# Kernel tuning notes

Measured on AMD Instinct MI355X. Metric: run time of the kernel, lower is better.

## Reference

```python
import jax, jax.numpy as jnp
import numpy as np
from jax.scipy.special import logsumexp

N_NODES = 20000
N_FEAT = 64
N_TPL = 10
TPL_NODES = 10
K_NEIGH = 15  # local neighborhood cap -> local graph size kloc = K+1 (self first)
N_EDGES = N_NODES * 16


def setup_inputs() -> dict:
    key = jax.random.key(0)
    k1, k2, k3, k4, k5 = jax.random.split(key, 5)
    x = jax.random.normal(k1, (N_NODES, N_FEAT), dtype=jnp.float32)
    edge_index = jax.random.randint(k2, (2, N_EDGES), 0, N_NODES, dtype=jnp.int32)
    # template_initialisation: randint{0,1} adjacency + N(0, 0.01) noise
    adj = jax.random.randint(k3, (N_TPL, TPL_NODES, TPL_NODES), 0, 2).astype(jnp.float32)
    templates = adj + 0.01 * jax.random.normal(k4, (N_TPL, TPL_NODES, TPL_NODES), dtype=jnp.float32)
    # template features ~ N(0.0012, 0.02)
    templates_features = 0.0012 + 0.02 * jax.random.normal(
        k5, (N_TPL, TPL_NODES, N_FEAT), dtype=jnp.float32)
    alpha0 = jnp.array([0.5], dtype=jnp.float32)
    return {"x": x, "edge_index": edge_index, "templates": templates,
            "templates_features": templates_features, "alpha0": alpha0}


def _fgw_distances(x, edge_index, templates, templates_features, alpha0,
                   K=K_NEIGH, n_outer=3, n_sink=5):
    """Per-node fused GW distance between the node's local (star) subgraph and
    each learned template, solved with an entropic proximal / Sinkhorn scheme.
    Returns [N, T]."""
    N, F = x.shape
    Tn, n, _ = templates.shape
    kloc = K + 1

    # ---- build fixed-size neighbor lists from edge_index (int ops, constant) ----
    src, dst = edge_index[0], edge_index[1]
    E = src.shape[0]
    order = jnp.argsort(src)
    src_s, dst_s = src[order], dst[order]
    deg = jnp.zeros((N,), jnp.int32).at[src].add(1)
    start = jnp.cumsum(deg) - deg                       # CSR row starts
    rank = jnp.arange(E, dtype=jnp.int32) - start[src_s]  # position within each node's list
    # rank >= K falls out of bounds -> dropped
    neigh = jnp.zeros((N, K), jnp.int32).at[src_s, rank].set(dst_s, mode="drop")
    nb_mask = (jnp.arange(K)[None, :] < jnp.minimum(deg, K)[:, None]).astype(x.dtype)  # [N,K]

    # ---- local graphs: self node first, then up to K neighbors ----
    xloc = jnp.concatenate([x[:, None, :], x[neigh]], axis=1)  # [N, kloc, F]
    m = jnp.concatenate([jnp.ones((N, 1), x.dtype), nb_mask], axis=1)  # [N, kloc]
    p = m / jnp.sum(m, -1, keepdims=True)                # node-side marginal
    q = jnp.full((n,), 1.0 / n, x.dtype)                 # template-side marginal

    # star adjacency of the 1-hop neighborhood
    row0 = jnp.concatenate([jnp.zeros((N, 1), x.dtype), nb_mask], axis=1)
    C1 = jnp.zeros((N, kloc, kloc), x.dtype).at[:, 0, :].set(row0).at[:, :, 0].set(row0)
    C2 = templates  # [T, n, n]

    # feature cost M[n_node, t, k, m] = ||xloc - y||^2
    M = (jnp.sum(xloc ** 2, -1)[:, None, :, None]
         + jnp.sum(templates_features ** 2, -1)[None, :, None, :]
         - 2.0 * jnp.einsum("nkf,tmf->ntkm", xloc, templates_features))

    alpha = jax.nn.sigmoid(alpha0)[0]

    # GW square-loss constant terms (Peyre et al. trick)
    hC1 = jnp.einsum("nkl,nl->nk", C1 ** 2, p)   # [N, kloc]
    hC2 = jnp.einsum("tmr,r->tm", C2 ** 2, q)    # [T, n]
    constC = hC1[:, None, :, None] + hC2[None, :, None, :]

    def gw_tens(Tp):  # Tp: [N, T, kloc, n]
        tmp = jnp.einsum("nkl,ntlm->ntkm", C1, Tp)
        return constC - 2.0 * jnp.einsum("ntkm,trm->ntkr", tmp, C2)

    eps = 0.05 * jax.lax.stop_gradient(jnp.mean(M)) + 1e-6
    logp = jnp.where(m > 0, jnp.log(jnp.maximum(p, 1e-30)), -1e9)[:, None, :]  # [N,1,kloc]
    logq = jnp.log(q)  # [n]

    Tp = p[:, None, :, None] * q[None, None, None, :]  # independent-coupling init
    f = jnp.zeros((N, Tn, kloc), x.dtype)
    g = jnp.zeros((N, Tn, n), x.dtype)
    for _ in range(n_outer):  # outer FGW linearization steps
        G = (1.0 - alpha) * M + 2.0 * alpha * gw_tens(Tp)
        logK = -G / eps
        for _ in range(n_sink):  # log-domain Sinkhorn on linearized cost
            f = eps * (logp - logsumexp(logK + g[:, :, None, :] / eps, axis=-1))
            g = eps * (logq - logsumexp(logK + f[:, :, :, None] / eps, axis=-2))
        Tp = jnp.exp(logK + f[:, :, :, None] / eps + g[:, :, None, :] / eps)

    dist = ((1.0 - alpha) * jnp.sum(M * Tp, axis=(-2, -1))
            + alpha * jnp.sum(gw_tens(Tp) * Tp, axis=(-2, -1)))
    return dist  # [N, T]


def reference(x, edge_index, templates, templates_features, alpha0):
    return _fgw_distances(x, edge_index, templates, templates_features, alpha0)
```

## Files before the change

kernel.cpp:

```cpp
#include <hip/hip_runtime.h>

#define N_NODES 20000
#define NPAIRS  10000
#define N_EDGES 320000
#define CAP     64
#define KN      15

typedef _Float16 half_t;
typedef _Float16 half2_t __attribute__((ext_vector_type(2)));

#define P_ALPHA 0
#define P_BETA  1
#define P_IEPS2 2
#define P_EPS   3
#define P_HC2   16
#define P_RSC2  216
#define P_F1    316

#define OFF_CNT    0u
#define OFF_S2X    80000u
#define OFF_STATS  160000u
#define OFF_FLAG   160520u
#define OFF_NBC    160528u
#define OFF_NEIGH  240528u
#define OFF_BUF    1440528u
#define OFF_PARAMS 6560528u
#define MEMSET_LEN 160528u

#define TF_STRIDE 648

template<int CTRL>
__device__ __forceinline__ float dpp_add(float v) {
  int s = __builtin_bit_cast(int, v);
  int r = __builtin_amdgcn_update_dpp(0, s, CTRL, 0xF, 0xF, true);
  return v + __builtin_bit_cast(float, r);
}
__device__ __forceinline__ float sum16(float v) {
  v = dpp_add<0x128>(v);
  v = dpp_add<0x124>(v);
  v = dpp_add<0x122>(v);
  v = dpp_add<0x121>(v);
  return v;
}
__device__ __forceinline__ float bcast16(float v) {
  return __builtin_bit_cast(float,
      __builtin_amdgcn_ds_swizzle(__builtin_bit_cast(int, v), 0x010));
}
__device__ __forceinline__ float fdot2(half2_t a, half2_t b, float c) {
  return __builtin_amdgcn_fdot2(a, b, c, false);
}
__device__ __forceinline__ float sgpr(float v) {
  return __builtin_bit_cast(float,
      __builtin_amdgcn_readfirstlane(__builtin_bit_cast(int, v)));
}

__global__ void k_scatter(const int* __restrict__ ei, int* __restrict__ cnt,
                          int* __restrict__ buf) {
  int e = blockIdx.x * blockDim.x + threadIdx.x;
  if (e >= N_EDGES) return;
  int s = ei[e];
  int slot = atomicAdd(&cnt[s], 1);
  if (slot < CAP) buf[s * CAP + slot] = e;
}

#define SS_BLOCKS 1250
__global__ void __launch_bounds__(256)
k_selstats(const int* __restrict__ ei, const int* __restrict__ cnt,
           const int* __restrict__ buf, const float* __restrict__ x,
           int* __restrict__ nbc_g, int* __restrict__ neigh,
           float* __restrict__ s2xh, double* __restrict__ stats,
           int* __restrict__ flag,
           const float* __restrict__ tf, const float* __restrict__ c2,
           const float* __restrict__ alpha0, float* __restrict__ params) {
  const int lane = threadIdx.x & 63;
  const int wid = threadIdx.x >> 6;
  const int* dst = ei + N_EDGES;
  const float x0 = x[lane];
  const float x0sq = x0 * x0;
  float accx = 0.f, acc2 = 0.f;
  __shared__ int dsh[4][16];

  for (int w = blockIdx.x * 4 + wid; w < N_NODES; w += SS_BLOCKS * 4) {
    int c = cnt[w];
    int cc = c < CAP ? c : CAP;
    int e = (lane < cc) ? buf[w * CAP + lane] : 0x7fffffff;
    int nb = c < KN ? c : KN;
    bool sel;
    if (cc <= KN) {
      sel = lane < cc;
    } else {
      int rank = 0;
      for (int j = 0; j < cc; j++) {
        int ej = __shfl(e, j);
        rank += (ej < e) ? 1 : 0;
      }
      sel = (e != 0x7fffffff) && (rank < KN);
    }
    unsigned long long mask = __ballot(sel);
    int d = sel ? dst[e] : 0;
    if (sel) {
      int pos = __popcll(mask & ((1ull << lane) - 1ull));
      neigh[w * KN + pos] = d;
      dsh[wid][pos] = d;
    }
    if (lane == 0) nbc_g[w] = nb;

    float sv = x[w * 64 + lane];
    {
      float hv = (float)(half_t)sv;
      float sq = hv * hv;
#pragma unroll
      for (int off = 32; off > 0; off >>= 1) sq += __shfl_xor(sq, off, 64);
      if (lane == 0) s2xh[w] = sq;
    }
    float ax = sv, a2 = sv * sv;
    int idx[KN];
#pragma unroll
    for (int r = 0; r < KN; r++) idx[r] = dsh[wid][r];
#pragma unroll
    for (int r = 0; r < KN; r++) {
      if (r < nb) {
        float nv = x[(size_t)idx[r] * 64 + lane];
        ax += nv;
        a2 = fmaf(nv, nv, a2);
      }
    }
    float w0 = (float)(KN - nb);
    ax = fmaf(w0, x0, ax);
    a2 = fmaf(w0, x0sq, a2);
    accx += ax;
    acc2 += a2;
  }

#pragma unroll
  for (int off = 32; off > 0; off >>= 1) acc2 += __shfl_xor(acc2, off, 64);
  __shared__ float redx[4][64];
  __shared__ float red2[4];
  __shared__ int lastsh;
  redx[wid][lane] = accx;
  if (lane == 0) red2[wid] = acc2;
  __syncthreads();
  int tid = threadIdx.x;
  if (tid < 64) {
    float s = redx[0][tid] + redx[1][tid] + redx[2][tid] + redx[3][tid];
    atomicAdd(&stats[1 + tid], (double)s);
  }
  if (tid == 0)
    atomicAdd(&stats[0], (double)(red2[0] + red2[1] + red2[2] + red2[3]));
  __syncthreads();
  if (tid == 0) {
    __threadfence();
    int old = atomicAdd(flag, 1);
    lastsh = (old == SS_BLOCKS - 1) ? 1 : 0;
  }
  __syncthreads();
  if (!lastsh) return;
  __threadfence();
  __shared__ float sh[4];
  if (tid < 64) {
    float s = 0.f, s2 = 0.f;
    for (int tm = 0; tm < 100; tm++) { float v = tf[tm * 64 + tid]; s += v; s2 += v * v; }
    double inv16N = 1.0 / (double)(N_NODES * 16);
    double cross = (stats[1 + tid] * inv16N) * ((double)s / 100.0);
    double B = (double)s2 / 100.0;
    double term = B - 2.0 * cross;
#pragma unroll
    for (int off = 32; off > 0; off >>= 1) term += __shfl_xor(term, off, 64);
    if (tid == 0) {
      double A = stats[0] * inv16N;
      double meanM = A + term;
      float eps = (float)(0.05 * meanM) + 1e-6f;
      float a0 = alpha0[0];
      float alpha = 1.f / (1.f + expf(-a0));
      params[P_ALPHA] = alpha;
      params[P_BETA]  = 1.f - alpha;
      params[P_IEPS2] = 1.4426950408889634f / eps;
      params[P_EPS]   = eps;
      sh[0] = alpha; sh[1] = 1.f - alpha; sh[2] = 1.4426950408889634f / eps;
    }
  }
  __syncthreads();
  if (tid < 100) {
    float alpha = sh[0], beta = sh[1], ieps2 = sh[2];
    int t = tid / 10, mm = tid % 10;
    float h = 0.f;
    for (int r = 0; r < 10; r++) { float cv = c2[t * 100 + mm * 10 + r]; h += cv * cv; }
    float hc2v = 0.1f * h;
    params[P_HC2 + tid] = hc2v;
    float s2 = 0.f;
    for (int f = 0; f < 64; f++) { float v = tf[tid * 64 + f]; s2 += v * v; }
    float rs = 0.f;
    for (int m2_ = 0; m2_ < 10; m2_++) rs += c2[t * 100 + mm * 10 + m2_];
    params[P_RSC2 + tid] = rs;
    params[P_F1 + tid] = (beta * s2 + 2.0f * alpha * hc2v) * (-ieps2);
  }
}

__global__ void __launch_bounds__(320, 6)
k_main(const float* __restrict__ x, const float* __restrict__ tf_g,
       const float* __restrict__ c2_g, const int* __restrict__ nbc_g,
       const int* __restrict__ neigh_g, const float* __restrict__ params,
       const float* __restrict__ s2x_g, float* __restrict__ out) {
  __shared__ __align__(16) half_t tf_l[10 * TF_STRIDE];
  __shared__ __align__(16) float c2_l[1000];
  __shared__ __align__(16) float hc2_l[100];
  __shared__ __align__(16) float rsc2_l[100];
  __shared__ __align__(16) float F1_l[100];
  __shared__ __align__(16) float bsb_l[20][10][2];

  const int tid = threadIdx.x;
  const int node_s = tid / 160;
  const int s = tid % 160;
  const int t = s >> 4;
  const int k = s & 15;
  const bool k0 = (k == 0);
  const int grp = node_s * 10 + t;

  for (int i = tid; i < 6400; i += 320) {
    int tt = i / 640, rem = i - tt * 640;
    tf_l[tt * TF_STRIDE + rem] = (half_t)tf_g[i];
  }
  for (int i = tid; i < 1000; i += 320) c2_l[i] = c2_g[i];
  if (tid < 100) {
    hc2_l[tid]  = params[P_HC2 + tid];
    rsc2_l[tid] = params[P_RSC2 + tid];
    F1_l[tid]   = params[P_F1 + tid];
  }

  const float alpha = sgpr(params[P_ALPHA]);
  const float beta  = sgpr(params[P_BETA]);
  const float ieps2 = sgpr(params[P_IEPS2]);
  const float eps   = sgpr(params[P_EPS]);
  const float niep  = -ieps2;
  const float twoal = 2.0f * alpha;
  const float ctv10 = 0.2f * twoal * ieps2;
  const float cab   = 2.0f * beta * ieps2;
  const float c_a2d = -eps * 0.69314718056f;
  const float twoal01 = 0.1f * twoal;

  const int idx_c2 = t * 100 + ((k < 10) ? k : 9) * 10;
  __syncthreads();

  const int kk = (k == 0) ? 0 : (k - 1);
  int p = blockIdx.x;
  int nb_pf = nbc_g[2 * p + node_s];
  int nbr_pf = neigh_g[(2 * p + node_s) * KN + kk];

#pragma unroll 1
  for (; p < NPAIRS; p += gridDim.x) {
    const int v = 2 * p + node_s;
    const int nb = nb_pf;
    const int srcn = (k == 0) ? v : (kk < nb ? nbr_pf : 0);
    const float s2x = s2x_g[srcn];
    const float4* xr = (const float4*)(x + (size_t)srcn * 64);

    {
      int vn = 2 * (p + gridDim.x) + node_s;
      vn = vn < N_NODES ? vn : 0;
      nb_pf = nbc_g[vn];
      nbr_pf = neigh_g[vn * KN + kk];
    }

    float acc[10];
#pragma unroll
    for (int m = 0; m < 10; m++) acc[m] = 0.0f;
    {
      const half_t* tfb = &tf_l[t * TF_STRIDE];
#pragma unroll 1
      for (int ch = 0; ch < 4; ch++) {
        float4 f0 = xr[ch * 4 + 0];
        float4 f1 = xr[ch * 4 + 1];
        float4 f2 = xr[ch * 4 + 2];
        float4 f3 = xr[ch * 4 + 3];
        half2_t x0 = { (half_t)f0.x, (half_t)f0.y };
        half2_t x1 = { (half_t)f0.z, (half_t)f0.w };
        half2_t x2 = { (half_t)f1.x, (half_t)f1.y };
        half2_t x3 = { (half_t)f1.z, (half_t)f1.w };
        half2_t x4 = { (half_t)f2.x, (half_t)f2.y };
        half2_t x5 = { (half_t)f2.z, (half_t)f2.w };
        half2_t x6 = { (half_t)f3.x, (half_t)f3.y };
        half2_t x7 = { (half_t)f3.z, (half_t)f3.w };
#pragma unroll
        for (int m = 0; m < 10; m++) {
          uint4 tqa = *(const uint4*)&tfb[m * 64 + ch * 16];
          uint4 tqb = *(const uint4*)&tfb[m * 64 + ch * 16 + 8];
          float a = acc[m];
          a = fdot2(__builtin_bit_cast(half2_t, tqa.x), x0, a);
          a = fdot2(__builtin_bit_cast(half2_t, tqa.y), x1, a);
          a = fdot2(__builtin_bit_cast(half2_t, tqa.z), x2, a);
          a = fdot2(__builtin_bit_cast(half2_t, tqa.w), x3, a);
          a = fdot2(__builtin_bit_cast(half2_t, tqb.x), x4, a);
          a = fdot2(__builtin_bit_cast(half2_t, tqb.y), x5, a);
          a = fdot2(__builtin_bit_cast(half2_t, tqb.z), x6, a);
          a = fdot2(__builtin_bit_cast(half2_t, tqb.w), x7, a);
          acc[m] = a;
        }
      }
    }

    const float inv = 1.0f / (float)(1 + nb);
    const float pk = (k <= nb) ? inv : 0.0f;
    const float hC1k = (k == 0) ? (float)nb * inv : ((k <= nb) ? inv : 0.0f);
    const float base = (beta * s2x + twoal * hC1k) * niep;
    const float ctm  = ctv10 * ((k == 0) ? (float)nb * inv : inv);

    float Ab[10];
#pragma unroll
    for (int j = 0; j < 5; j++) {
      float2 f1v = *(const float2*)&F1_l[t * 10 + 2 * j];
      Ab[2 * j]     = fmaf(cab, acc[2 * j],     f1v.x + base);
      Ab[2 * j + 1] = fmaf(cab, acc[2 * j + 1], f1v.y + base);
    }

    float K[10], vv[10];
    float u = 1.0f;
#pragma unroll
    for (int m = 0; m < 10; m++) vv[m] = 1.0f;

#pragma unroll
    for (int j = 0; j < 5; j++) {
      float2 rs = *(const float2*)&rsc2_l[t * 10 + 2 * j];
      K[2 * j]     = __builtin_amdgcn_exp2f(fmaf(ctm, rs.x, Ab[2 * j]));
      K[2 * j + 1] = __builtin_amdgcn_exp2f(fmaf(ctm, rs.y, Ab[2 * j + 1]));
    }

#pragma unroll 1
    for (int o = 0; o < 3; o++) {
#pragma unroll 1
      for (int it = 0; it < 5; it++) {
        float kv0 = 0.0f, kv1 = 0.0f;
#pragma unroll
        for (int m = 0; m < 10; m += 2) {
          kv0 = fmaf(K[m],     vv[m],     kv0);
          kv1 = fmaf(K[m + 1], vv[m + 1], kv1);
        }
        u = pk * __builtin_amdgcn_rcpf(kv0 + kv1);
#pragma unroll
        for (int m = 0; m < 10; m++) {
          float w = sum16(K[m] * u);
          vv[m] = __builtin_amdgcn_rcpf(w);
        }
      }
      if (o == 2) break;
      {
        float B = 0.0f, SB = 0.0f;
#pragma unroll
        for (int j = 0; j < 5; j++) {
          float2 c2p = *(const float2*)&c2_l[idx_c2 + 2 * j];
          float tka = K[2 * j] * vv[2 * j] * u;
          float tkb = K[2 * j + 1] * vv[2 * j + 1] * u;
          B  = fmaf(bcast16(tka), c2p.x, B);
          SB = fmaf(sum16(tka),   c2p.x, SB);
          B  = fmaf(bcast16(tkb), c2p.y, B);
          SB = fmaf(sum16(tkb),   c2p.y, SB);
        }
        if (k < 10) { bsb_l[grp][k][0] = B; bsb_l[grp][k][1] = SB; }
        __threadfence_block();
#pragma unroll
        for (int j = 0; j < 5; j++) {
          float4 bv = *(const float4*)&bsb_l[grp][2 * j][0];
          float tva = k0 ? (bv.y - bv.x) : bv.x;
          float tvb = k0 ? (bv.w - bv.z) : bv.z;
          K[2 * j]     = __builtin_amdgcn_exp2f(fmaf(ctv10, tva, Ab[2 * j]));
          K[2 * j + 1] = __builtin_amdgcn_exp2f(fmaf(ctv10, tvb, Ab[2 * j + 1]));
        }
        __threadfence_block();
      }
    }

    {
      float tk[10];
      float B = 0.0f, SB = 0.0f;
#pragma unroll
      for (int j = 0; j < 5; j++) {
        float2 c2p = *(const float2*)&c2_l[idx_c2 + 2 * j];
        tk[2 * j]     = K[2 * j] * vv[2 * j] * u;
        tk[2 * j + 1] = K[2 * j + 1] * vv[2 * j + 1] * u;
        B  = fmaf(bcast16(tk[2 * j]), c2p.x, B);
        SB = fmaf(sum16(tk[2 * j]),   c2p.x, SB);
        B  = fmaf(bcast16(tk[2 * j + 1]), c2p.y, B);
        SB = fmaf(sum16(tk[2 * j + 1]),   c2p.y, SB);
      }
      if (k < 10) { bsb_l[grp][k][0] = B; bsb_l[grp][k][1] = SB; }
      __threadfence_block();
      float dd = 0.0f;
#pragma unroll
      for (int j = 0; j < 5; j++) {
        float4 bv = *(const float4*)&bsb_l[grp][2 * j][0];
        float2 h2 = *(const float2*)&hc2_l[t * 10 + 2 * j];
        float tva = k0 ? (bv.y - bv.x) : bv.x;
        float tvb = k0 ? (bv.w - bv.z) : bv.z;
        float c1a = fmaf(alpha, hC1k + h2.x, twoal01 * tva);
        float c1b = fmaf(alpha, hC1k + h2.y, twoal01 * tvb);
        float coa = fmaf(c_a2d, Ab[2 * j], -c1a);
        float cob = fmaf(c_a2d, Ab[2 * j + 1], -c1b);
        dd = fmaf(coa, tk[2 * j], dd);
        dd = fmaf(cob, tk[2 * j + 1], dd);
      }
      __threadfence_block();
      dd = sum16(dd * 0.1f);
      if (k == 0) out[v * 10 + t] = dd;
    }
  }
}

extern "C" void kernel_launch(void* const* d_in, const int* in_sizes, int n_in,
                              void* d_out, int out_size, void* d_ws, size_t ws_size,
                              hipStream_t stream) {
  const float* x  = (const float*)d_in[0];
  const int*   ei = (const int*)d_in[1];
  const float* c2 = (const float*)d_in[2];
  const float* tf = (const float*)d_in[3];
  const float* a0 = (const float*)d_in[4];
  float* out = (float*)d_out;
  char* ws = (char*)d_ws;
  int*    cnt    = (int*)(ws + OFF_CNT);
  float*  s2xh   = (float*)(ws + OFF_S2X);
  double* stats  = (double*)(ws + OFF_STATS);
  int*    flag   = (int*)(ws + OFF_FLAG);
  int*    nbc    = (int*)(ws + OFF_NBC);
  int*    neigh  = (int*)(ws + OFF_NEIGH);
  int*    buf    = (int*)(ws + OFF_BUF);
  float*  params = (float*)(ws + OFF_PARAMS);
  (void)in_sizes; (void)n_in; (void)out_size; (void)ws_size;

  hipMemsetAsync(ws, 0, MEMSET_LEN, stream);
  k_scatter<<<N_EDGES / 256, 256, 0, stream>>>(ei, cnt, buf);
  k_selstats<<<SS_BLOCKS, 256, 0, stream>>>(ei, cnt, buf, x, nbc, neigh,
                                            s2xh, stats, flag, tf, c2, a0, params);
  k_main<<<2500, 320, 0, stream>>>(x, tf, c2, nbc, neigh, params, s2xh, out);
}
```

Measured before the change: 402.3 us.

## Software-pipeline next node's feature loads and dot products into Sinkhorn phases

```diff
diff --git a/kernel.cpp b/kernel.cpp
--- a/kernel.cpp
+++ b/kernel.cpp
@@ -5,6 +5,7 @@
 #define N_EDGES 320000
 #define CAP     64
 #define KN      15
+#define GRID_MAIN 2500
 
 typedef _Float16 half_t;
 typedef _Float16 half2_t __attribute__((ext_vector_type(2)));
@@ -196,7 +197,46 @@
   }
 }
 
-__global__ void __launch_bounds__(320, 6)
+struct XChunk { float4 a, b, c, d; };
+
+__device__ __forceinline__ XChunk ld_chunk(const float4* __restrict__ xr, int ch) {
+  XChunk f;
+  f.a = xr[ch * 4 + 0];
+  f.b = xr[ch * 4 + 1];
+  f.c = xr[ch * 4 + 2];
+  f.d = xr[ch * 4 + 3];
+  return f;
+}
+
+__device__ __forceinline__ void fdot_chunk(const XChunk& f,
+                                           const half_t* __restrict__ tfb,
+                                           int ch, float acc[10]) {
+  half2_t x0 = { (half_t)f.a.x, (half_t)f.a.y };
+  half2_t x1 = { (half_t)f.a.z, (half_t)f.a.w };
+  half2_t x2 = { (half_t)f.b.x, (half_t)f.b.y };
+  half2_t x3 = { (half_t)f.b.z, (half_t)f.b.w };
+  half2_t x4 = { (half_t)f.c.x, (half_t)f.c.y };
+  half2_t x5 = { (half_t)f.c.z, (half_t)f.c.w };
+  half2_t x6 = { (half_t)f.d.x, (half_t)f.d.y };
+  half2_t x7 = { (half_t)f.d.z, (half_t)f.d.w };
+#pragma unroll
+  for (int m = 0; m < 10; m++) {
+    uint4 tqa = *(const uint4*)&tfb[m * 64 + ch * 16];
+    uint4 tqb = *(const uint4*)&tfb[m * 64 + ch * 16 + 8];
+    float a = acc[m];
+    a = fdot2(__builtin_bit_cast(half2_t, tqa.x), x0, a);
+    a = fdot2(__builtin_bit_cast(half2_t, tqa.y), x1, a);
+    a = fdot2(__builtin_bit_cast(half2_t, tqa.z), x2, a);
+    a = fdot2(__builtin_bit_cast(half2_t, tqa.w), x3, a);
+    a = fdot2(__builtin_bit_cast(half2_t, tqb.x), x4, a);
+    a = fdot2(__builtin_bit_cast(half2_t, tqb.y), x5, a);
+    a = fdot2(__builtin_bit_cast(half2_t, tqb.z), x6, a);
+    a = fdot2(__builtin_bit_cast(half2_t, tqb.w), x7, a);
+    acc[m] = a;
+  }
+}
+
+__global__ void __launch_bounds__(320, 5)
 k_main(const float* __restrict__ x, const float* __restrict__ tf_g,
        const float* __restrict__ c2_g, const int* __restrict__ nbc_g,
        const int* __restrict__ neigh_g, const float* __restrict__ params,
@@ -215,6 +255,13 @@
   const int k = s & 15;
   const bool k0 = (k == 0);
   const int grp = node_s * 10 + t;
+  const int kk = (k == 0) ? 0 : (k - 1);
+
+  const int v0 = 2 * blockIdx.x + node_s;
+  int nb_c  = nbc_g[v0];
+  int nbr_c = neigh_g[v0 * KN + kk];
+  int nb_n  = nbc_g[v0 + 2 * GRID_MAIN];
+  int nbr_n = neigh_g[(v0 + 2 * GRID_MAIN) * KN + kk];
 
   for (int i = tid; i < 6400; i += 320) {
     int tt = i / 640, rem = i - tt * 640;
@@ -241,75 +288,59 @@
   const int idx_c2 = t * 100 + ((k < 10) ? k : 9) * 10;
   __syncthreads();
 
-  const int kk = (k == 0) ? 0 : (k - 1);
-  int p = blockIdx.x;
-  int nb_pf = nbc_g[2 * p + node_s];
-  int nbr_pf = neigh_g[(2 * p + node_s) * KN + kk];
+  const half_t* tfb = &tf_l[t * TF_STRIDE];
+
+  int srcn_c = k0 ? v0 : (kk < nb_c ? nbr_c : 0);
+  float s2x_c = s2x_g[srcn_c];
+  float acc_c[10];
+#pragma unroll
+  for (int m = 0; m < 10; m++) acc_c[m] = 0.0f;
+  {
+    const float4* xr = (const float4*)(x + (size_t)srcn_c * 64);
+    XChunk f0 = ld_chunk(xr, 0);
+    XChunk f1 = ld_chunk(xr, 1);
+    XChunk f2 = ld_chunk(xr, 2);
+    XChunk f3 = ld_chunk(xr, 3);
+    fdot_chunk(f0, tfb, 0, acc_c);
+    fdot_chunk(f1, tfb, 1, acc_c);
+    fdot_chunk(f2, tfb, 2, acc_c);
+    fdot_chunk(f3, tfb, 3, acc_c);
+  }
 
 #pragma unroll 1
-  for (; p < NPAIRS; p += gridDim.x) {
-    const int v = 2 * p + node_s;
-    const int nb = nb_pf;
-    const int srcn = (k == 0) ? v : (kk < nb ? nbr_pf : 0);
-    const float s2x = s2x_g[srcn];
-    const float4* xr = (const float4*)(x + (size_t)srcn * 64);
-
-    {
-      int vn = 2 * (p + gridDim.x) + node_s;
-      vn = vn < N_NODES ? vn : 0;
-      nb_pf = nbc_g[vn];
-      nbr_pf = neigh_g[vn * KN + kk];
-    }
-
-    float acc[10];
-#pragma unroll
-    for (int m = 0; m < 10; m++) acc[m] = 0.0f;
-    {
-      const half_t* tfb = &tf_l[t * TF_STRIDE];
-#pragma unroll 1
-      for (int ch = 0; ch < 4; ch++) {
-        float4 f0 = xr[ch * 4 + 0];
-        float4 f1 = xr[ch * 4 + 1];
-        float4 f2 = xr[ch * 4 + 2];
-        float4 f3 = xr[ch * 4 + 3];
-        half2_t x0 = { (half_t)f0.x, (half_t)f0.y };
-        half2_t x1 = { (half_t)f0.z, (half_t)f0.w };
-        half2_t x2 = { (half_t)f1.x, (half_t)f1.y };
-        half2_t x3 = { (half_t)f1.z, (half_t)f1.w };
-        half2_t x4 = { (half_t)f2.x, (half_t)f2.y };
-        half2_t x5 = { (half_t)f2.z, (half_t)f2.w };
-        half2_t x6 = { (half_t)f3.x, (half_t)f3.y };
-        half2_t x7 = { (half_t)f3.z, (half_t)f3.w };
-#pragma unroll
-        for (int m = 0; m < 10; m++) {
-          uint4 tqa = *(const uint4*)&tfb[m * 64 + ch * 16];
-          uint4 tqb = *(const uint4*)&tfb[m * 64 + ch * 16 + 8];
-          float a = acc[m];
-          a = fdot2(__builtin_bit_cast(half2_t, tqa.x), x0, a);
-          a = fdot2(__builtin_bit_cast(half2_t, tqa.y), x1, a);
-          a = fdot2(__builtin_bit_cast(half2_t, tqa.z), x2, a);
-          a = fdot2(__builtin_bit_cast(half2_t, tqa.w), x3, a);
-          a = fdot2(__builtin_bit_cast(half2_t, tqb.x), x4, a);
-          a = fdot2(__builtin_bit_cast(half2_t, tqb.y), x5, a);
-          a = fdot2(__builtin_bit_cast(half2_t, tqb.z), x6, a);
-          a = fdot2(__builtin_bit_cast(half2_t, tqb.w), x7, a);
-          acc[m] = a;
-        }
-      }
-    }
-
+  for (int i = 0; i < 4; i++) {
+    const int v = 2 * (blockIdx.x + i * GRID_MAIN) + node_s;
+    const bool notlast = (i < 3);
+
+    XChunk cf;
+    const float4* xrn = (const float4*)x;
+    float s2x_n = 0.0f;
+    if (notlast) {
+      int srcn_n = k0 ? (v + 2 * GRID_MAIN) : (kk < nb_n ? nbr_n : 0);
+      xrn = (const float4*)(x + (size_t)srcn_n * 64);
+      cf = ld_chunk(xrn, 0);
+      s2x_n = s2x_g[srcn_n];
+    }
+    int nb_n2 = 0, nbr_n2 = 0;
+    if (i < 2) {
+      int v2 = v + 4 * GRID_MAIN;
+      nb_n2  = nbc_g[v2];
+      nbr_n2 = neigh_g[v2 * KN + kk];
+    }
+
+    const int nb = nb_c;
     const float inv = 1.0f / (float)(1 + nb);
     const float pk = (k <= nb) ? inv : 0.0f;
     const float hC1k = (k == 0) ? (float)nb * inv : ((k <= nb) ? inv : 0.0f);
-    const float base = (beta * s2x + twoal * hC1k) * niep;
+    const float base = (beta * s2x_c + twoal * hC1k) * niep;
     const float ctm  = ctv10 * ((k == 0) ? (float)nb * inv : inv);
 
     float Ab[10];
 #pragma unroll
     for (int j = 0; j < 5; j++) {
       float2 f1v = *(const float2*)&F1_l[t * 10 + 2 * j];
-      Ab[2 * j]     = fmaf(cab, acc[2 * j],     f1v.x + base);
-      Ab[2 * j + 1] = fmaf(cab, acc[2 * j + 1], f1v.y + base);
+      Ab[2 * j]     = fmaf(cab, acc_c[2 * j],     f1v.x + base);
+      Ab[2 * j + 1] = fmaf(cab, acc_c[2 * j + 1], f1v.y + base);
     }
 
     float K[10], vv[10];
@@ -324,8 +355,11 @@
       K[2 * j + 1] = __builtin_amdgcn_exp2f(fmaf(ctm, rs.y, Ab[2 * j + 1]));
     }
 
-#pragma unroll 1
-    for (int o = 0; o < 3; o++) {
+    float acc_n[10];
+#pragma unroll
+    for (int m = 0; m < 10; m++) acc_n[m] = 0.0f;
+
+    auto sink5 = [&]() {
 #pragma unroll 1
       for (int it = 0; it < 5; it++) {
         float kv0 = 0.0f, kv1 = 0.0f;
@@ -341,32 +375,41 @@
           vv[m] = __builtin_amdgcn_rcpf(w);
         }
       }
-      if (o == 2) break;
-      {
-        float B = 0.0f, SB = 0.0f;
-#pragma unroll
-        for (int j = 0; j < 5; j++) {
-          float2 c2p = *(const float2*)&c2_l[idx_c2 + 2 * j];
-          float tka = K[2 * j] * vv[2 * j] * u;
-          float tkb = K[2 * j + 1] * vv[2 * j + 1] * u;
-          B  = fmaf(bcast16(tka), c2p.x, B);
-          SB = fmaf(sum16(tka),   c2p.x, SB);
-          B  = fmaf(bcast16(tkb), c2p.y, B);
-          SB = fmaf(sum16(tkb),   c2p.y, SB);
-        }
-        if (k < 10) { bsb_l[grp][k][0] = B; bsb_l[grp][k][1] = SB; }
-        __threadfence_block();
-#pragma unroll
-        for (int j = 0; j < 5; j++) {
-          float4 bv = *(const float4*)&bsb_l[grp][2 * j][0];
-          float tva = k0 ? (bv.y - bv.x) : bv.x;
-          float tvb = k0 ? (bv.w - bv.z) : bv.z;
-          K[2 * j]     = __builtin_amdgcn_exp2f(fmaf(ctv10, tva, Ab[2 * j]));
-          K[2 * j + 1] = __builtin_amdgcn_exp2f(fmaf(ctv10, tvb, Ab[2 * j + 1]));
-        }
-        __threadfence_block();
-      }
-    }
+    };
+
+    auto site = [&]() {
+      float B = 0.0f, SB = 0.0f;
+#pragma unroll
+      for (int j = 0; j < 5; j++) {
+        float2 c2p = *(const float2*)&c2_l[idx_c2 + 2 * j];
+        float tka = K[2 * j] * vv[2 * j] * u;
+        float tkb = K[2 * j + 1] * vv[2 * j + 1] * u;
+        B  = fmaf(bcast16(tka), c2p.x, B);
+        SB = fmaf(sum16(tka),   c2p.x, SB);
+        B  = fmaf(bcast16(tkb), c2p.y, B);
+        SB = fmaf(sum16(tkb),   c2p.y, SB);
+      }
+      if (k < 10) { bsb_l[grp][k][0] = B; bsb_l[grp][k][1] = SB; }
+      __threadfence_block();
+#pragma unroll
+      for (int j = 0; j < 5; j++) {
+        float4 bv = *(const float4*)&bsb_l[grp][2 * j][0];
+        float tva = k0 ? (bv.y - bv.x) : bv.x;
+        float tvb = k0 ? (bv.w - bv.z) : bv.z;
+        K[2 * j]     = __builtin_amdgcn_exp2f(fmaf(ctv10, tva, Ab[2 * j]));
+        K[2 * j + 1] = __builtin_amdgcn_exp2f(fmaf(ctv10, tvb, Ab[2 * j + 1]));
+      }
+      __threadfence_block();
+    };
+
+    sink5();
+    if (notlast) { fdot_chunk(cf, tfb, 0, acc_n); cf = ld_chunk(xrn, 1); }
+    site();
+    sink5();
+    if (notlast) { fdot_chunk(cf, tfb, 1, acc_n); cf = ld_chunk(xrn, 2); }
+    site();
+    sink5();
+    if (notlast) { fdot_chunk(cf, tfb, 2, acc_n); cf = ld_chunk(xrn, 3); }
 
     {
       float tk[10];
@@ -401,6 +444,12 @@
       dd = sum16(dd * 0.1f);
       if (k == 0) out[v * 10 + t] = dd;
     }
+
+    if (notlast) { fdot_chunk(cf, tfb, 3, acc_n); }
+    nb_c  = nb_n;  s2x_c = s2x_n;
+    nb_n  = nb_n2; nbr_n = nbr_n2;
+#pragma unroll
+    for (int m = 0; m < 10; m++) acc_c[m] = acc_n[m];
   }
 }
 
@@ -428,5 +477,5 @@
   k_scatter<<<N_EDGES / 256, 256, 0, stream>>>(ei, cnt, buf);
   k_selstats<<<SS_BLOCKS, 256, 0, stream>>>(ei, cnt, buf, x, nbc, neigh,
                                             s2xh, stats, flag, tf, c2, a0, params);
-  k_main<<<2500, 320, 0, stream>>>(x, tf, c2, nbc, neigh, params, s2xh, out);
-}
+  k_main<<<GRID_MAIN, 320, 0, stream>>>(x, tf, c2, nbc, neigh, params, s2xh, out);
+}
```

After: 406.9 us. Within noise of the previous version (+1.1%).
